# Optimization experiments

Hardware: AMD Instinct MI355X
Metric: run time of the kernel (lower is better)

Reference implementation:

```python
import jax, jax.numpy as jnp
import numpy as np

D_MODEL = 2048
N_HEADS = 32
N_KV_HEADS = 8
ROPE_BASE = 10000.0


def setup_inputs() -> dict:
    key = jax.random.key(0)
    ks = jax.random.split(key, 5)
    b, s, d = 2, 2048, D_MODEL
    hd = d // N_HEADS
    scale = 0.02
    return {
        "x": jax.random.normal(ks[0], (b, s, d), jnp.float32),
        "wq": jax.random.normal(ks[1], (N_HEADS * hd, d), jnp.float32) * scale,
        "wk": jax.random.normal(ks[2], (N_KV_HEADS * hd, d), jnp.float32) * scale,
        "wv": jax.random.normal(ks[3], (N_KV_HEADS * hd, d), jnp.float32) * scale,
        "wo": jax.random.normal(ks[4], (d, N_HEADS * hd), jnp.float32) * scale,
    }


def _rope_cos_sin(seq_len, head_dim):
    # theta_j = base^(-2j/d); freqs[i, j] = i * theta_j; repeat-interleave x2 on last dim
    theta = 1.0 / (ROPE_BASE ** (jnp.arange(0, head_dim, 2, dtype=jnp.float32) / head_dim))
    freqs = jnp.arange(seq_len, dtype=jnp.float32)[:, None] * theta[None, :]  # [S, hd/2]
    cos = jnp.repeat(jnp.cos(freqs), 2, axis=-1)[None, :, None, :]  # [1, S, 1, hd]
    sin = jnp.repeat(jnp.sin(freqs), 2, axis=-1)[None, :, None, :]
    return cos, sin


def _rotate(t):
    # interleaved rotate-half: (x0, x1, x2, x3, ...) -> (-x1, x0, -x3, x2, ...)
    t1 = t[..., ::2]
    t2 = t[..., 1::2]
    return jnp.stack([-t2, t1], axis=-1).reshape(t.shape)


def reference(x, wq, wk, wv, wo):
    b, s, d = x.shape
    hd = d // N_HEADS
    n_rep = N_HEADS // N_KV_HEADS

    q = (x @ wq.T).reshape(b, s, N_HEADS, hd)       # [b, s, H, hd]
    k = (x @ wk.T).reshape(b, s, N_KV_HEADS, hd)    # [b, s, G, hd]
    v = (x @ wv.T).reshape(b, s, N_KV_HEADS, hd)

    cos, sin = _rope_cos_sin(s, hd)
    q = q * cos + _rotate(q) * sin
    k = k * cos + _rotate(k) * sin

    # GQA without physical KV replication: group query heads by shared KV head.
    # repeat_interleave(n_rep, dim=2) maps kv head g -> query heads [g*n_rep, (g+1)*n_rep)
    qg = q.reshape(b, s, N_KV_HEADS, n_rep, hd)
    scale = 1.0 / jnp.sqrt(jnp.asarray(hd, q.dtype))
    scores = jnp.einsum('bqgrd,bkgd->bgrqk', qg, k) * scale  # [b, G, rep, Sq, Sk]

    causal = jnp.tril(jnp.ones((s, s), dtype=bool))
    scores = jnp.where(causal[None, None, None], scores, jnp.asarray(-jnp.inf, scores.dtype))
    attn = jax.nn.softmax(scores, axis=-1)

    out = jnp.einsum('bgrqk,bkgd->bqgrd', attn, v).reshape(b, s, N_HEADS * hd)
    return out @ wo.T
```

## Files before the change

kernel.cpp:

```cpp
#include <hip/hip_runtime.h>

typedef unsigned short u16;
typedef __attribute__((ext_vector_type(8))) short bf16x8;
typedef __attribute__((ext_vector_type(4))) float f32x4;

#define LOG2E 1.44269504088896340736f

__device__ inline u16 f2b(float f) {
    unsigned int u = __builtin_bit_cast(unsigned int, f);
    unsigned int r = u + 0x7fffu + ((u >> 16) & 1u);
    return (u16)(r >> 16);
}
__device__ inline float b2f(u16 h) {
    unsigned int u = ((unsigned int)h) << 16;
    return __builtin_bit_cast(float, u);
}

#define GLOAD_LDS16(g, l) \
    __builtin_amdgcn_global_load_lds( \
        (const __attribute__((address_space(1))) unsigned int*)(g), \
        (__attribute__((address_space(3))) unsigned int*)(l), 16, 0, 0)

__global__ __launch_bounds__(256) void cast_all(
    const float* __restrict__ x, const float* __restrict__ wq,
    const float* __restrict__ wk, const float* __restrict__ wv,
    const float* __restrict__ wo, u16* __restrict__ xb,
    u16* __restrict__ wqkvb, u16* __restrict__ wob) {
    long i = ((long)blockIdx.x * 256 + threadIdx.x) * 4;
    const float* s;
    u16* d;
    if (i < 8388608)       { s = x  + i;              d = xb + i; }
    else if (i < 12582912) { s = wq + (i - 8388608);  d = wqkvb + (i - 8388608); }
    else if (i < 13631488) { s = wk + (i - 12582912); d = wqkvb + 4194304 + (i - 12582912); }
    else if (i < 14680064) { s = wv + (i - 13631488); d = wqkvb + 5242880 + (i - 13631488); }
    else                   { s = wo + (i - 14680064); d = wob + (i - 14680064); }
    float4 v = *(const float4*)s;
    ushort4 o = make_ushort4(f2b(v.x), f2b(v.y), f2b(v.z), f2b(v.w));
    *(ushort4*)d = o;
}

__global__ __launch_bounds__(256) void rope_kernel(u16* __restrict__ qkv, float qscale) {
    int idx = blockIdx.x * 256 + threadIdx.x;
    int row = idx / 320;
    int rem = idx - row * 320;
    int head = rem >> 3, chunk = rem & 7;
    int pos = row & 2047;
    int coloff;
    float scale;
    if (head < 32) { coloff = head * 64;               scale = qscale; }
    else           { coloff = 2048 + (head - 32) * 64; scale = 1.0f; }
    u16* p = qkv + (size_t)row * 3072 + coloff + chunk * 8;
    bf16x8 v = *(bf16x8*)p;
    float t0 = exp2f((float)(chunk * 4) * -0.41524101186092f);
    const float tc[4] = {1.0f, 0.74989420933246f, 0.56234132519035f, 0.42169650342858f};
    float fpos = (float)pos;
    #pragma unroll
    for (int i = 0; i < 4; i++) {
        float f = fpos * (t0 * tc[i]);
        float rev = f * 0.15915494309189535f;
        rev = rev - floorf(rev);
        float sn = __builtin_amdgcn_sinf(rev);
        float cs = __builtin_amdgcn_cosf(rev);
        float e0 = b2f((u16)v[2 * i]), e1 = b2f((u16)v[2 * i + 1]);
        v[2 * i]     = (short)f2b((e0 * cs - e1 * sn) * scale);
        v[2 * i + 1] = (short)f2b((e1 * cs + e0 * sn) * scale);
    }
    *(bf16x8*)p = v;
}

__global__ __launch_bounds__(256) void vtrans_kernel(
    const u16* __restrict__ QKV, u16* __restrict__ VT) {
    const int S = 2048, RS = 3072;
    int b = blockIdx.z, g = blockIdx.y, st = blockIdx.x;
    __shared__ u16 T[64 * 72];
    int tid = threadIdx.x;
    for (int c = tid; c < 512; c += 256) {
        int sr = c >> 3, dc = (c & 7) * 8;
        *(bf16x8*)&T[sr * 72 + dc] =
            *(const bf16x8*)(QKV + ((size_t)b * S + st * 64 + sr) * RS + 2560 + g * 64 + dc);
    }
    __syncthreads();
    for (int c = tid; c < 512; c += 256) {
        int d = c >> 3, sc = (c & 7) * 8;
        bf16x8 o;
        #pragma unroll
        for (int j = 0; j < 8; j++) o[j] = (short)T[(sc + j) * 72 + d];
        *(bf16x8*)(VT + ((size_t)((b * 8 + g) * 64 + d)) * S + st * 64 + sc) = o;
    }
}

__global__ __launch_bounds__(256) void gemm_bt128(
    const u16* __restrict__ A, const u16* __restrict__ B, void* __restrict__ Cv,
    int M, int N, int K, int c_is_f32) {
    __shared__ u16 As[128 * 32];
    __shared__ u16 Bs[128 * 32];
    const int tid = threadIdx.x;
    const int lane = tid & 63, wave = tid >> 6;
    const int ln = lane & 15, quad = lane >> 4;
    const int wm = wave >> 1, wn = wave & 1;
    const int m0 = blockIdx.y * 128, n0 = blockIdx.x * 128;

    const int srow = wave * 16 + (lane >> 2);
    const int skc = (lane & 3) * 8;
    const u16* Ag = A + (size_t)(m0 + srow) * K + skc;
    const u16* Bg = B + (size_t)(n0 + srow) * K + skc;

    f32x4 acc[4][4] = {};
    for (int k0 = 0; k0 < K; k0 += 32) {
        #pragma unroll
        for (int t = 0; t < 2; t++) {
            GLOAD_LDS16(Ag + (size_t)t * 64 * K + k0, As + t * 2048 + wave * 512);
            GLOAD_LDS16(Bg + (size_t)t * 64 * K + k0, Bs + t * 2048 + wave * 512);
        }
        __syncthreads();

        bf16x8 af[4], bfr[4];
        #pragma unroll
        for (int i = 0; i < 4; i++) {
            af[i]  = *(const bf16x8*)&As[(wm * 64 + i * 16 + ln) * 32 + quad * 8];
            bfr[i] = *(const bf16x8*)&Bs[(wn * 64 + i * 16 + ln) * 32 + quad * 8];
        }
        #pragma unroll
        for (int mi = 0; mi < 4; mi++)
            #pragma unroll
            for (int nt = 0; nt < 4; nt++)
                acc[mi][nt] = __builtin_amdgcn_mfma_f32_16x16x32_bf16(
                    af[mi], bfr[nt], acc[mi][nt], 0, 0, 0);
        __syncthreads();
    }

    #pragma unroll
    for (int mi = 0; mi < 4; mi++)
        #pragma unroll
        for (int nt = 0; nt < 4; nt++)
            #pragma unroll
            for (int r = 0; r < 4; r++) {
                int row = m0 + wm * 64 + mi * 16 + quad * 4 + r;
                int col = n0 + wn * 64 + nt * 16 + ln;
                float v = acc[mi][nt][r];
                if (c_is_f32) ((float*)Cv)[(size_t)row * N + col] = v;
                else          ((u16*)Cv)[(size_t)row * N + col] = f2b(v);
            }
}

__global__ __launch_bounds__(256) void attn_kernel(
    const u16* __restrict__ QKV, const u16* __restrict__ VT, u16* __restrict__ O) {
    const int S = 2048, RS = 3072, DO = 2048;
    const int b = blockIdx.z, h = blockIdx.y, p = blockIdx.x;
    const int g = h >> 2;
    const int qtl = p, qth = (S / 64 - 1) - p;
    const int tid = threadIdx.x;
    const int lane = tid & 63, wave = tid >> 6;
    const int ln = lane & 15, quad = lane >> 4;

    __shared__ u16 Ks[64 * 72];
    __shared__ u16 Vt[64 * 72];
    __shared__ u16 Ps[64 * 72];

    const u16* Qb = QKV + (size_t)b * S * RS + h * 64 + quad * 8;
    bf16x8 aqh0 = *(const bf16x8*)(Qb + (size_t)(qth * 64 + wave * 16 + ln) * RS);
    bf16x8 aqh1 = *(const bf16x8*)(Qb + (size_t)(qth * 64 + wave * 16 + ln) * RS + 32);
    bf16x8 aql0 = *(const bf16x8*)(Qb + (size_t)(qtl * 64 + wave * 16 + ln) * RS);
    bf16x8 aql1 = *(const bf16x8*)(Qb + (size_t)(qtl * 64 + wave * 16 + ln) * RS + 32);

    const u16* Kb = QKV + (size_t)b * S * RS + 2048 + g * 64;
    const u16* VTb = VT + (size_t)(b * 8 + g) * 64 * S;

    const bf16x8 vones = {0x3F80, 0x3F80, 0x3F80, 0x3F80, 0x3F80, 0x3F80, 0x3F80, 0x3F80};

    f32x4 acch[5] = {}, accl[5] = {};

    const int r0 = tid >> 3;
    const int dc0 = (tid & 7) * 8;
    bf16x8 kreg0, kreg1, vreg0, vreg1;
    auto loadKV = [&](int kt) {
        kreg0 = *(const bf16x8*)(Kb + (size_t)(kt * 64 + r0) * RS + dc0);
        kreg1 = *(const bf16x8*)(Kb + (size_t)(kt * 64 + r0 + 32) * RS + dc0);
        vreg0 = *(const bf16x8*)(VTb + (size_t)r0 * S + kt * 64 + dc0);
        vreg1 = *(const bf16x8*)(VTb + (size_t)(r0 + 32) * S + kt * 64 + dc0);
    };

    auto process = [&](int qt, bf16x8 aq0, bf16x8 aq1, f32x4* acco, int kt) {
        f32x4 accs[4] = {};
        #pragma unroll
        for (int nt = 0; nt < 4; nt++) {
            bf16x8 bk0 = *(const bf16x8*)&Ks[(nt * 16 + ln) * 72 + quad * 8];
            accs[nt] = __builtin_amdgcn_mfma_f32_16x16x32_bf16(aq0, bk0, accs[nt], 0, 0, 0);
            bf16x8 bk1 = *(const bf16x8*)&Ks[(nt * 16 + ln) * 72 + 32 + quad * 8];
            accs[nt] = __builtin_amdgcn_mfma_f32_16x16x32_bf16(aq1, bk1, accs[nt], 0, 0, 0);
        }

        if (kt == qt) {
            #pragma unroll
            for (int nt = 0; nt < 4; nt++)
                #pragma unroll
                for (int r = 0; r < 4; r++) {
                    int kidx = nt * 16 + ln;
                    int qidx = wave * 16 + quad * 4 + r;
                    if (kidx > qidx) accs[nt][r] = -INFINITY;
                }
        }

        #pragma unroll
        for (int nt = 0; nt < 4; nt++)
            #pragma unroll
            for (int r = 0; r < 4; r++) {
                float pv = exp2f(accs[nt][r]);
                Ps[(wave * 16 + quad * 4 + r) * 72 + nt * 16 + ln] =
                    (u16)(__builtin_bit_cast(unsigned int, pv) >> 16);
            }

        #pragma unroll
        for (int kk = 0; kk < 2; kk++) {
            bf16x8 ap = *(const bf16x8*)&Ps[(wave * 16 + ln) * 72 + kk * 32 + quad * 8];
            #pragma unroll
            for (int nt = 0; nt < 4; nt++) {
                bf16x8 bv = *(const bf16x8*)&Vt[(nt * 16 + ln) * 72 + kk * 32 + quad * 8];
                acco[nt] = __builtin_amdgcn_mfma_f32_16x16x32_bf16(ap, bv, acco[nt], 0, 0, 0);
            }
            acco[4] = __builtin_amdgcn_mfma_f32_16x16x32_bf16(ap, vones, acco[4], 0, 0, 0);
        }
    };

    loadKV(0);
    for (int kt = 0; kt <= qth; kt++) {
        __syncthreads();
        *(bf16x8*)&Ks[r0 * 72 + dc0] = kreg0;
        *(bf16x8*)&Ks[(r0 + 32) * 72 + dc0] = kreg1;
        *(bf16x8*)&Vt[r0 * 72 + dc0] = vreg0;
        *(bf16x8*)&Vt[(r0 + 32) * 72 + dc0] = vreg1;
        __syncthreads();
        if (kt < qth) loadKV(kt + 1);

        process(qth, aqh0, aqh1, acch, kt);
        if (kt <= qtl)
            process(qtl, aql0, aql1, accl, kt);
    }

    u16* Ob = O + (size_t)b * S * DO + h * 64;
    #pragma unroll
    for (int r = 0; r < 4; r++) {
        float invh = 1.0f / acch[4][r];
        float invl = 1.0f / accl[4][r];
        int qh = qth * 64 + wave * 16 + quad * 4 + r;
        int ql = qtl * 64 + wave * 16 + quad * 4 + r;
        #pragma unroll
        for (int nt = 0; nt < 4; nt++) {
            Ob[(size_t)qh * DO + nt * 16 + ln] = f2b(acch[nt][r] * invh);
            Ob[(size_t)ql * DO + nt * 16 + ln] = f2b(accl[nt][r] * invl);
        }
    }
}

extern "C" void kernel_launch(void* const* d_in, const int* in_sizes, int n_in,
                              void* d_out, int out_size, void* d_ws, size_t ws_size,
                              hipStream_t stream) {
    const float* x  = (const float*)d_in[0];
    const float* wq = (const float*)d_in[1];
    const float* wk = (const float*)d_in[2];
    const float* wv = (const float*)d_in[3];
    const float* wo = (const float*)d_in[4];

    const int B = 2, S = 2048, D = 2048, H = 32, KVH = 8;
    const int M = B * S;
    const int NQKV = 3072;

    char* ws = (char*)d_ws;
    size_t off = 0;
    auto alloc = [&](size_t bytes) {
        void* p = ws + off;
        off += (bytes + 255) & ~(size_t)255;
        return p;
    };
    u16* xb    = (u16*)alloc((size_t)M * D * 2);
    u16* wqkvb = (u16*)alloc((size_t)NQKV * D * 2);
    u16* wob   = (u16*)alloc((size_t)D * D * 2);
    u16* QKV   = (u16*)alloc((size_t)M * NQKV * 2);
    u16* AO = xb;
    u16* VT = wqkvb;

    cast_all<<<dim3(18432), 256, 0, stream>>>(x, wq, wk, wv, wo, xb, wqkvb, wob);

    gemm_bt128<<<dim3(NQKV / 128, M / 128), 256, 0, stream>>>(xb, wqkvb, QKV, M, NQKV, D, 0);

    const float sscale = 0.125f * LOG2E;
    rope_kernel<<<dim3(M * 320 / 256), 256, 0, stream>>>(QKV, sscale);

    vtrans_kernel<<<dim3(S / 64, KVH, B), 256, 0, stream>>>(QKV, VT);

    attn_kernel<<<dim3(S / 128, H, B), 256, 0, stream>>>(QKV, VT, AO);

    gemm_bt128<<<dim3(D / 128, M / 128), 256, 0, stream>>>(AO, wob, d_out, M, D, D, 1);
}
```

Baseline: 342.2 us.

## Interleave high and low query tiles in attention loop; widen cast to 8 elements

The attention kernel now handles both query tiles in one fused loop body. Each K fragment loaded from shared memory is reused for the MFMAs of both tiles, and each V fragment is likewise shared by both PV MFMAs, giving the scheduler independent MFMA chains to interleave. Separate P buffers with a 68-element stride let both tiles' probabilities sit in LDS at once, at the cost of slightly more shared memory and register pressure. The cast kernel also processes 8 elements per thread with half as many blocks.

Result: slower. 354.8 us (+3.7%).

```diff
diff --git a/kernel.cpp b/kernel.cpp
--- a/kernel.cpp
+++ b/kernel.cpp
@@ -26,7 +26,7 @@
     const float* __restrict__ wk, const float* __restrict__ wv,
     const float* __restrict__ wo, u16* __restrict__ xb,
     u16* __restrict__ wqkvb, u16* __restrict__ wob) {
-    long i = ((long)blockIdx.x * 256 + threadIdx.x) * 4;
+    long i = ((long)blockIdx.x * 256 + threadIdx.x) * 8;
     const float* s;
     u16* d;
     if (i < 8388608)       { s = x  + i;              d = xb + i; }
@@ -34,9 +34,12 @@
     else if (i < 13631488) { s = wk + (i - 12582912); d = wqkvb + 4194304 + (i - 12582912); }
     else if (i < 14680064) { s = wv + (i - 13631488); d = wqkvb + 5242880 + (i - 13631488); }
     else                   { s = wo + (i - 14680064); d = wob + (i - 14680064); }
-    float4 v = *(const float4*)s;
-    ushort4 o = make_ushort4(f2b(v.x), f2b(v.y), f2b(v.z), f2b(v.w));
-    *(ushort4*)d = o;
+    float4 v0 = *(const float4*)s;
+    float4 v1 = *(const float4*)(s + 4);
+    ushort4 o0 = make_ushort4(f2b(v0.x), f2b(v0.y), f2b(v0.z), f2b(v0.w));
+    ushort4 o1 = make_ushort4(f2b(v1.x), f2b(v1.y), f2b(v1.z), f2b(v1.w));
+    *(ushort4*)d = o0;
+    *(ushort4*)(d + 4) = o1;
 }
 
 __global__ __launch_bounds__(256) void rope_kernel(u16* __restrict__ qkv, float qscale) {
@@ -155,7 +158,8 @@
 
     __shared__ u16 Ks[64 * 72];
     __shared__ u16 Vt[64 * 72];
-    __shared__ u16 Ps[64 * 72];
+    __shared__ u16 Psh[64 * 68];
+    __shared__ u16 Psl[64 * 68];
 
     const u16* Qb = QKV + (size_t)b * S * RS + h * 64 + quad * 8;
     bf16x8 aqh0 = *(const bf16x8*)(Qb + (size_t)(qth * 64 + wave * 16 + ln) * RS);
@@ -180,48 +184,6 @@
         vreg1 = *(const bf16x8*)(VTb + (size_t)(r0 + 32) * S + kt * 64 + dc0);
     };
 
-    auto process = [&](int qt, bf16x8 aq0, bf16x8 aq1, f32x4* acco, int kt) {
-        f32x4 accs[4] = {};
-        #pragma unroll
-        for (int nt = 0; nt < 4; nt++) {
-            bf16x8 bk0 = *(const bf16x8*)&Ks[(nt * 16 + ln) * 72 + quad * 8];
-            accs[nt] = __builtin_amdgcn_mfma_f32_16x16x32_bf16(aq0, bk0, accs[nt], 0, 0, 0);
-            bf16x8 bk1 = *(const bf16x8*)&Ks[(nt * 16 + ln) * 72 + 32 + quad * 8];
-            accs[nt] = __builtin_amdgcn_mfma_f32_16x16x32_bf16(aq1, bk1, accs[nt], 0, 0, 0);
-        }
-
-        if (kt == qt) {
-            #pragma unroll
-            for (int nt = 0; nt < 4; nt++)
-                #pragma unroll
-                for (int r = 0; r < 4; r++) {
-                    int kidx = nt * 16 + ln;
-                    int qidx = wave * 16 + quad * 4 + r;
-                    if (kidx > qidx) accs[nt][r] = -INFINITY;
-                }
-        }
-
-        #pragma unroll
-        for (int nt = 0; nt < 4; nt++)
-            #pragma unroll
-            for (int r = 0; r < 4; r++) {
-                float pv = exp2f(accs[nt][r]);
-                Ps[(wave * 16 + quad * 4 + r) * 72 + nt * 16 + ln] =
-                    (u16)(__builtin_bit_cast(unsigned int, pv) >> 16);
-            }
-
-        #pragma unroll
-        for (int kk = 0; kk < 2; kk++) {
-            bf16x8 ap = *(const bf16x8*)&Ps[(wave * 16 + ln) * 72 + kk * 32 + quad * 8];
-            #pragma unroll
-            for (int nt = 0; nt < 4; nt++) {
-                bf16x8 bv = *(const bf16x8*)&Vt[(nt * 16 + ln) * 72 + kk * 32 + quad * 8];
-                acco[nt] = __builtin_amdgcn_mfma_f32_16x16x32_bf16(ap, bv, acco[nt], 0, 0, 0);
-            }
-            acco[4] = __builtin_amdgcn_mfma_f32_16x16x32_bf16(ap, vones, acco[4], 0, 0, 0);
-        }
-    };
-
     loadKV(0);
     for (int kt = 0; kt <= qth; kt++) {
         __syncthreads();
@@ -232,9 +194,71 @@
         __syncthreads();
         if (kt < qth) loadKV(kt + 1);
 
-        process(qth, aqh0, aqh1, acch, kt);
-        if (kt <= qtl)
-            process(qtl, aql0, aql1, accl, kt);
+        const bool dual = (kt <= qtl);
+
+        f32x4 sh[4] = {}, sl[4] = {};
+        #pragma unroll
+        for (int nt = 0; nt < 4; nt++) {
+            bf16x8 bk0 = *(const bf16x8*)&Ks[(nt * 16 + ln) * 72 + quad * 8];
+            bf16x8 bk1 = *(const bf16x8*)&Ks[(nt * 16 + ln) * 72 + 32 + quad * 8];
+            sh[nt] = __builtin_amdgcn_mfma_f32_16x16x32_bf16(aqh0, bk0, sh[nt], 0, 0, 0);
+            sh[nt] = __builtin_amdgcn_mfma_f32_16x16x32_bf16(aqh1, bk1, sh[nt], 0, 0, 0);
+            if (dual) {
+                sl[nt] = __builtin_amdgcn_mfma_f32_16x16x32_bf16(aql0, bk0, sl[nt], 0, 0, 0);
+                sl[nt] = __builtin_amdgcn_mfma_f32_16x16x32_bf16(aql1, bk1, sl[nt], 0, 0, 0);
+            }
+        }
+
+        if (kt == qth) {
+            #pragma unroll
+            for (int nt = 0; nt < 4; nt++)
+                #pragma unroll
+                for (int r = 0; r < 4; r++)
+                    if (nt * 16 + ln > wave * 16 + quad * 4 + r) sh[nt][r] = -INFINITY;
+        }
+        #pragma unroll
+        for (int nt = 0; nt < 4; nt++)
+            #pragma unroll
+            for (int r = 0; r < 4; r++) {
+                float pv = exp2f(sh[nt][r]);
+                Psh[(wave * 16 + quad * 4 + r) * 68 + nt * 16 + ln] =
+                    (u16)(__builtin_bit_cast(unsigned int, pv) >> 16);
+            }
+        if (dual) {
+            if (kt == qtl) {
+                #pragma unroll
+                for (int nt = 0; nt < 4; nt++)
+                    #pragma unroll
+                    for (int r = 0; r < 4; r++)
+                        if (nt * 16 + ln > wave * 16 + quad * 4 + r) sl[nt][r] = -INFINITY;
+            }
+            #pragma unroll
+            for (int nt = 0; nt < 4; nt++)
+                #pragma unroll
+                for (int r = 0; r < 4; r++) {
+                    float pv = exp2f(sl[nt][r]);
+                    Psl[(wave * 16 + quad * 4 + r) * 68 + nt * 16 + ln] =
+                        (u16)(__builtin_bit_cast(unsigned int, pv) >> 16);
+                }
+        }
+
+        #pragma unroll
+        for (int kk = 0; kk < 2; kk++) {
+            bf16x8 aph = *(const bf16x8*)&Psh[(wave * 16 + ln) * 68 + kk * 32 + quad * 8];
+            bf16x8 apl;
+            if (dual)
+                apl = *(const bf16x8*)&Psl[(wave * 16 + ln) * 68 + kk * 32 + quad * 8];
+            #pragma unroll
+            for (int nt = 0; nt < 4; nt++) {
+                bf16x8 bv = *(const bf16x8*)&Vt[(nt * 16 + ln) * 72 + kk * 32 + quad * 8];
+                acch[nt] = __builtin_amdgcn_mfma_f32_16x16x32_bf16(aph, bv, acch[nt], 0, 0, 0);
+                if (dual)
+                    accl[nt] = __builtin_amdgcn_mfma_f32_16x16x32_bf16(apl, bv, accl[nt], 0, 0, 0);
+            }
+            acch[4] = __builtin_amdgcn_mfma_f32_16x16x32_bf16(aph, vones, acch[4], 0, 0, 0);
+            if (dual)
+                accl[4] = __builtin_amdgcn_mfma_f32_16x16x32_bf16(apl, vones, accl[4], 0, 0, 0);
+        }
     }
 
     u16* Ob = O + (size_t)b * S * DO + h * 64;
@@ -279,7 +303,7 @@
     u16* AO = xb;
     u16* VT = wqkvb;
 
-    cast_all<<<dim3(18432), 256, 0, stream>>>(x, wq, wk, wv, wo, xb, wqkvb, wob);
+    cast_all<<<dim3(9216), 256, 0, stream>>>(x, wq, wk, wv, wo, xb, wqkvb, wob);
 
     gemm_bt128<<<dim3(NQKV / 128, M / 128), 256, 0, stream>>>(xb, wqkvb, QKV, M, NQKV, D, 0);
 
```
